# Kernel tuning notes

Measured on AMD Instinct MI355X. Metric: run time of the kernel, lower is better.

Reference implementation:

```python
import jax, jax.numpy as jnp
import numpy as np

B, T, E = 2, 2048, 1024   # batch, block_size, emb_d
H, D = 16, 64             # heads, head_size


def setup_inputs() -> dict:
    key = jax.random.key(0)
    ks = jax.random.split(key, 7)
    s = 1.0 / np.sqrt(E)
    inputs = jax.random.normal(ks[0], (B, T, E), dtype=jnp.float32)
    k_w = jax.random.uniform(ks[1], (H, E, D), jnp.float32, -s, s)
    k_b = jax.random.uniform(ks[2], (H, D), jnp.float32, -s, s)
    q_w = jax.random.uniform(ks[3], (H, E, D), jnp.float32, -s, s)
    q_b = jax.random.uniform(ks[4], (H, D), jnp.float32, -s, s)
    v_w = jax.random.uniform(ks[5], (H, E, D), jnp.float32, -s, s)
    v_b = jax.random.uniform(ks[6], (H, D), jnp.float32, -s, s)
    return {"inputs": inputs, "k_w": k_w, "k_b": k_b,
            "q_w": q_w, "q_b": q_b, "v_w": v_w, "v_b": v_b}


def reference(inputs, k_w, k_b, q_w, q_b, v_w, v_b):
    # Per-head linear projections, vectorized over heads: (B,T,E)x(H,E,D)->(B,H,T,D)
    k = jnp.einsum('bte,hed->bhtd', inputs, k_w) + k_b[None, :, None, :]
    q = jnp.einsum('bte,hed->bhtd', inputs, q_w) + q_b[None, :, None, :]
    v = jnp.einsum('bte,hed->bhtd', inputs, v_w) + v_b[None, :, None, :]

    scale = D ** (-0.5)
    # scores: (B,H,Tq,Tk)
    w = jnp.einsum('bhtd,bhsd->bhts', q, k) * scale
    tril = jnp.tril(jnp.ones((T, T), dtype=bool))
    w = jnp.where(tril[None, None, :, :], w, -jnp.inf)
    # NOTE: original torch code does softmax(weights, dim=1) on a (B,T,T)
    # tensor, i.e. over the QUERY axis. Faithfully reproduce: axis=-2 here.
    w = jax.nn.softmax(w, axis=-2)
    out = jnp.einsum('bhts,bhsd->bhtd', w, v)           # (B,H,T,D)
    # concat heads along last dim, head-major order matching torch.cat
    return out.transpose(0, 2, 1, 3).reshape(B, T, H * D)
```

## Files before the change

kernel.cpp:

```cpp
#include <hip/hip_runtime.h>
#include <hip/hip_bf16.h>
#include <math.h>

#define B_ 2
#define T_ 2048
#define E_ 1024
#define H_ 16
#define D_ 64
#define NT_ 32
#define QSCALE 0.180336880f

typedef __attribute__((ext_vector_type(8))) short bf16x8;
typedef __attribute__((ext_vector_type(4))) float f32x4;

#if __has_builtin(__builtin_amdgcn_exp2f)
#define EXP2(x) __builtin_amdgcn_exp2f(x)
#else
#define EXP2(x) exp2f(x)
#endif

__device__ __forceinline__ unsigned short f2bf(float x) {
  union { float f; unsigned u; } v; v.f = x;
  unsigned r = v.u + 0x7FFFu + ((v.u >> 16) & 1u);
  return (unsigned short)(r >> 16);
}
__device__ __forceinline__ unsigned pk2bf(float a, float b) {
  __hip_bfloat162 h = __float22bfloat162_rn(make_float2(a, b));
  union { __hip_bfloat162 h; unsigned u; } c; c.h = h; return c.u;
}

__device__ __forceinline__ void dma8(const unsigned short* g, int gstride,
                                     unsigned short* l, int lane)
{
  const int r = lane >> 3, bg = (lane & 7) ^ (r & 7);
  __builtin_amdgcn_global_load_lds(
      (const __attribute__((address_space(1))) void*)(g + (size_t)r * gstride + bg * 8),
      (__attribute__((address_space(3))) void*)l, 16, 0, 0);
}
__device__ __forceinline__ bf16x8 frag(const unsigned short* tile, int row, int g) {
  return *(const bf16x8*)(tile + row * 64 + (((g ^ row) & 7) << 3));
}

__global__ __launch_bounds__(256) void pack_kernel(
    const float* __restrict__ in, unsigned short* __restrict__ o16,
    const float* __restrict__ qw, const float* __restrict__ kw, const float* __restrict__ vw,
    unsigned short* __restrict__ qwt, unsigned short* __restrict__ kwt,
    unsigned short* __restrict__ vwt)
{
  __shared__ float s[64][65];
  const int tid = threadIdx.x;
  if (blockIdx.x < 2048) {
    const size_t i = ((size_t)blockIdx.x * 256 + tid) * 8;
    float4 f0 = *(const float4*)(in + i);
    float4 f1 = *(const float4*)(in + i + 4);
    unsigned u[4] = { pk2bf(f0.x, f0.y), pk2bf(f0.z, f0.w),
                      pk2bf(f1.x, f1.y), pk2bf(f1.z, f1.w) };
    *(bf16x8*)(o16 + i) = *(const bf16x8*)u;
    return;
  }
  const int i = blockIdx.x - 2048;
  const int e0 = (i & 15) * 64, h = (i >> 4) & 15, z = i >> 8;
  const float* w = (z == 0) ? qw : (z == 1) ? kw : vw;
  unsigned short* o = (z == 0) ? qwt : (z == 1) ? kwt : vwt;
  {
    const int r = tid >> 2;
    #pragma unroll
    for (int p = 0; p < 4; ++p) {
      const int c = (tid & 3) * 4 + p * 16;
      float4 f = *(const float4*)(w + ((size_t)(h * E_ + e0 + r)) * D_ + c);
      s[r][c] = f.x; s[r][c+1] = f.y; s[r][c+2] = f.z; s[r][c+3] = f.w;
    }
  }
  __syncthreads();
  {
    const int d = tid >> 2, ec = (tid & 3) * 16;
    unsigned short tmp[16];
    #pragma unroll
    for (int j = 0; j < 16; ++j) tmp[j] = f2bf(s[ec + j][d]);
    unsigned short* dst = o + ((size_t)(h * D_ + d)) * E_ + e0 + ec;
    *(bf16x8*)(dst)     = *(const bf16x8*)&tmp[0];
    *(bf16x8*)(dst + 8) = *(const bf16x8*)&tmp[8];
  }
}

__global__ __launch_bounds__(256) void proj_kernel(
    const unsigned short* __restrict__ in16,
    const unsigned short* __restrict__ qwt, const unsigned short* __restrict__ kwt,
    const unsigned short* __restrict__ vwt,
    const float* __restrict__ qb, const float* __restrict__ kb, const float* __restrict__ vb,
    unsigned short* __restrict__ qo, unsigned short* __restrict__ ko,
    unsigned short* __restrict__ vt)
{
  __shared__ __align__(16) unsigned short in_s[2][128 * 64];
  __shared__ __align__(16) unsigned short w_s[2][3 * 64 * 64];
  const int tid = threadIdx.x;
  const int lane = tid & 63, wv = tid >> 6;
  const int l15 = lane & 15, quad = lane >> 4;
  const int t0 = blockIdx.x * 128, h = blockIdx.y, b = blockIdx.z;
  const int bh = b * H_ + h;
  const unsigned short* wts[3] = { qwt, kwt, vwt };

  f32x4 acc[3][8];
  #pragma unroll
  for (int x = 0; x < 3; ++x)
    #pragma unroll
    for (int tb = 0; tb < 8; ++tb) acc[x][tb] = (f32x4){0.f, 0.f, 0.f, 0.f};

#define PROJ_STAGE(e0_, bi_)                                                      \
  {                                                                               \
    const unsigned short* gin = in16 + ((size_t)(b * T_ + t0)) * E_ + (e0_);      \
    _Pragma("unroll")                                                             \
    for (int p = 0; p < 4; ++p) {                                                 \
      const int br = wv * 32 + p * 8;                                             \
      dma8(gin + (size_t)br * E_, E_, &in_s[bi_][br * 64], lane);                 \
    }                                                                             \
    _Pragma("unroll")                                                             \
    for (int j = 0; j < 6; ++j) {                                                 \
      const int idx = wv * 6 + j;                                                 \
      const int x = idx >> 3, br = (idx & 7) * 8;                                 \
      dma8(wts[x] + ((size_t)(h * D_ + br)) * E_ + (e0_), E_,                     \
           &w_s[bi_][x * 4096 + br * 64], lane);                                  \
    }                                                                             \
  }

  PROJ_STAGE(0, 0);
  __syncthreads();
  for (int e = 0; e < 16; ++e) {
    const int bi = e & 1;
    if (e < 15) PROJ_STAGE((e + 1) * 64, bi ^ 1);
    const unsigned short* is = in_s[bi];
    const unsigned short* ws = w_s[bi];
    #pragma unroll
    for (int kk = 0; kk < 2; ++kk) {
      const int g0 = kk * 4 + quad;
      bf16x8 bfr[3];
      #pragma unroll
      for (int x = 0; x < 3; ++x)
        bfr[x] = frag(ws, x * 64 + wv * 16 + l15, g0);
      bf16x8 afr[8];
      #pragma unroll
      for (int tb = 0; tb < 8; ++tb)
        afr[tb] = frag(is, tb * 16 + l15, g0);
      #pragma unroll
      for (int tb = 0; tb < 8; ++tb) {
        acc[0][tb] = __builtin_amdgcn_mfma_f32_16x16x32_bf16(bfr[0], afr[tb], acc[0][tb], 0, 0, 0);
        acc[1][tb] = __builtin_amdgcn_mfma_f32_16x16x32_bf16(bfr[1], afr[tb], acc[1][tb], 0, 0, 0);
        acc[2][tb] = __builtin_amdgcn_mfma_f32_16x16x32_bf16(afr[tb], bfr[2], acc[2][tb], 0, 0, 0);
      }
    }
    __syncthreads();
  }
#undef PROJ_STAGE

  const size_t obase = (size_t)bh * T_;
  #pragma unroll
  for (int x = 0; x < 2; ++x) {
    const float scl = (x == 0) ? QSCALE : 1.0f;
    const float* bias = (x == 0) ? qb : kb;
    unsigned short* outp = (x == 0) ? qo : ko;
    float bias4[4];
    *(float4*)bias4 = *(const float4*)&bias[h * D_ + wv * 16 + quad * 4];
    #pragma unroll
    for (int tb = 0; tb < 8; ++tb) {
      const int t = t0 + tb * 16 + l15;
      unsigned short pk[4];
      #pragma unroll
      for (int r = 0; r < 4; ++r) pk[r] = f2bf((acc[x][tb][r] + bias4[r]) * scl);
      *(ushort4*)(outp + (obase + t) * D_ + wv * 16 + quad * 4) = *(const ushort4*)pk;
    }
  }
  {
    const int d = wv * 16 + l15;
    const float bvv = vb[h * D_ + d];
    #pragma unroll
    for (int tb = 0; tb < 8; ++tb) {
      const int t = t0 + tb * 16 + quad * 4;
      unsigned short pk[4];
      #pragma unroll
      for (int r = 0; r < 4; ++r) pk[r] = f2bf(acc[2][tb][r] + bvv);
      *(ushort4*)(vt + ((size_t)(bh * D_ + d)) * T_ + t) = *(const ushort4*)pk;
    }
  }
}

__global__ __launch_bounds__(256) void stats_kernel(
    const unsigned short* __restrict__ q, const unsigned short* __restrict__ k,
    float* __restrict__ lg)
{
  __shared__ __align__(16) unsigned short q_s[2][64 * 64];
  __shared__ float red[4][64];
  const int tid = threadIdx.x;
  const int lane = tid & 63, wv = tid >> 6;
  const int l15 = lane & 15, quad = lane >> 4;
  const int h = blockIdx.x, b = blockIdx.y, sa = blockIdx.z;
  const int bh = b * H_ + h;
  const int s0 = sa * 64;
  const unsigned short* qbase = q + (size_t)bh * T_ * 64;

  bf16x8 kf[4][2];
  #pragma unroll
  for (int nb = 0; nb < 4; ++nb)
    #pragma unroll
    for (int kk = 0; kk < 2; ++kk)
      kf[nb][kk] = *(const bf16x8*)(k + ((size_t)(bh * T_ + s0 + nb * 16 + l15)) * 64
                                      + kk * 32 + quad * 8);

  #pragma unroll
  for (int pp = 0; pp < 2; ++pp) {
    const int br = wv * 16 + pp * 8;
    dma8(qbase + (size_t)(sa * 64 + br) * 64, 64, &q_s[0][br * 64], lane);
  }
  __syncthreads();

  float lsum[4] = {0.f, 0.f, 0.f, 0.f};

  for (int tt = sa, i = 0; tt < NT_; ++tt, ++i) {
    const int bi = i & 1;
    if (tt + 1 < NT_) {
      #pragma unroll
      for (int pp = 0; pp < 2; ++pp) {
        const int br = wv * 16 + pp * 8;
        dma8(qbase + (size_t)((tt + 1) * 64 + br) * 64, 64, &q_s[bi ^ 1][br * 64], lane);
      }
    }
    bf16x8 a0 = frag(q_s[bi], wv * 16 + l15, quad);
    bf16x8 a1 = frag(q_s[bi], wv * 16 + l15, 4 + quad);
    f32x4 sacc[4];
    #pragma unroll
    for (int nb = 0; nb < 4; ++nb) sacc[nb] = (f32x4){0.f, 0.f, 0.f, 0.f};
    #pragma unroll
    for (int nb = 0; nb < 4; ++nb) {
      sacc[nb] = __builtin_amdgcn_mfma_f32_16x16x32_bf16(a0, kf[nb][0], sacc[nb], 0, 0, 0);
      sacc[nb] = __builtin_amdgcn_mfma_f32_16x16x32_bf16(a1, kf[nb][1], sacc[nb], 0, 0, 0);
    }
    if (tt == sa) {
      const int tbase = tt * 64 + wv * 16 + quad * 4;
      #pragma unroll
      for (int nb = 0; nb < 4; ++nb) {
        const int s = s0 + nb * 16 + l15;
        #pragma unroll
        for (int r = 0; r < 4; ++r)
          lsum[nb] += (tbase + r >= s) ? EXP2(sacc[nb][r]) : 0.f;
      }
    } else {
      #pragma unroll
      for (int nb = 0; nb < 4; ++nb)
        #pragma unroll
        for (int r = 0; r < 4; ++r) lsum[nb] += EXP2(sacc[nb][r]);
    }
    __syncthreads();
  }
  #pragma unroll
  for (int nb = 0; nb < 4; ++nb) {
    lsum[nb] += __shfl_xor(lsum[nb], 16);
    lsum[nb] += __shfl_xor(lsum[nb], 32);
  }
  if (lane < 16) {
    #pragma unroll
    for (int nb = 0; nb < 4; ++nb) red[wv][nb * 16 + lane] = lsum[nb];
  }
  __syncthreads();
  if (tid < 64) {
    const float L = red[0][tid] + red[1][tid] + red[2][tid] + red[3][tid];
    lg[(size_t)bh * T_ + s0 + tid] = -__log2f(L);
  }
}

__global__ __launch_bounds__(256) void out_kernel(
    const unsigned short* __restrict__ q, const unsigned short* __restrict__ k,
    const unsigned short* __restrict__ vt, const float* __restrict__ lg,
    float* __restrict__ out)
{
  __shared__ __align__(16) unsigned short k_s[2][64 * 64];
  __shared__ __align__(16) unsigned short vt_s[2][64 * 64];
  __shared__ __align__(16) unsigned short u_s[4][32][40];
  __shared__ float lg_sh[2][64];
  const int tid = threadIdx.x;
  const int lane = tid & 63, wv = tid >> 6;
  const int l15 = lane & 15, quad = lane >> 4;
  const int th = wv >> 1, sh = wv & 1;
  const int h = blockIdx.x, b = blockIdx.y, jt = 31 - blockIdx.z;
  const int bh = b * H_ + h;
  const int t0 = jt * 64;
  const unsigned short* kbase = k + (size_t)bh * T_ * 64;
  const unsigned short* vbase = vt + (size_t)bh * D_ * T_;
  const float* lgbase = lg + (size_t)bh * T_;

  bf16x8 qf[2][2];
  #pragma unroll
  for (int nt = 0; nt < 2; ++nt) {
    const unsigned short* qrow = q + (size_t)(bh * T_ + t0 + th * 32 + nt * 16 + l15) * 64;
    qf[nt][0] = *(const bf16x8*)(qrow + quad * 8);
    qf[nt][1] = *(const bf16x8*)(qrow + 32 + quad * 8);
  }

  #pragma unroll
  for (int pp = 0; pp < 2; ++pp) {
    const int br = wv * 16 + pp * 8;
    dma8(kbase + (size_t)br * 64, 64, &k_s[0][br * 64], lane);
    dma8(vbase + (size_t)br * T_, T_, &vt_s[0][br * 64], lane);
  }
  if (tid < 64) lg_sh[0][tid] = lgbase[tid];
  __syncthreads();

  f32x4 oacc[4][2];
  #pragma unroll
  for (int mb = 0; mb < 4; ++mb)
    #pragma unroll
    for (int nt = 0; nt < 2; ++nt) oacc[mb][nt] = (f32x4){0.f, 0.f, 0.f, 0.f};

  for (int st = 0; st <= jt; ++st) {
    const int bi = st & 1;
    if (st < jt) {
      const int s1 = (st + 1) * 64;
      #pragma unroll
      for (int pp = 0; pp < 2; ++pp) {
        const int br = wv * 16 + pp * 8;
        dma8(kbase + (size_t)(s1 + br) * 64, 64, &k_s[bi ^ 1][br * 64], lane);
        dma8(vbase + (size_t)br * T_ + s1, T_, &vt_s[bi ^ 1][br * 64], lane);
      }
      if (tid < 64) lg_sh[bi ^ 1][tid] = lgbase[s1 + tid];
    }
    const unsigned short* ks = k_s[bi];
    const unsigned short* vs = vt_s[bi];
    const float* lgb = lg_sh[bi];

    const bool dead = (st == jt) && (th == 0) && (sh == 1);
    if (!dead) {
      f32x4 sacc[2][2];
      #pragma unroll
      for (int mb = 0; mb < 2; ++mb) {
        float lg4[4];
        *(float4*)lg4 = *(const float4*)&lgb[sh * 32 + mb * 16 + quad * 4];
        #pragma unroll
        for (int nt = 0; nt < 2; ++nt)
          sacc[mb][nt] = (f32x4){lg4[0], lg4[1], lg4[2], lg4[3]};
      }
      #pragma unroll
      for (int mb = 0; mb < 2; ++mb) {
        bf16x8 ka0 = frag(ks, sh * 32 + mb * 16 + l15, quad);
        bf16x8 ka1 = frag(ks, sh * 32 + mb * 16 + l15, 4 + quad);
        #pragma unroll
        for (int nt = 0; nt < 2; ++nt) {
          sacc[mb][nt] = __builtin_amdgcn_mfma_f32_16x16x32_bf16(ka0, qf[nt][0], sacc[mb][nt], 0, 0, 0);
          sacc[mb][nt] = __builtin_amdgcn_mfma_f32_16x16x32_bf16(ka1, qf[nt][1], sacc[mb][nt], 0, 0, 0);
        }
      }
      const bool diagmask = (st == jt) && (th == sh);
      #pragma unroll
      for (int mb = 0; mb < 2; ++mb)
        #pragma unroll
        for (int nt = 0; nt < 2; ++nt) {
          float uu[4] = { EXP2(sacc[mb][nt][0]), EXP2(sacc[mb][nt][1]),
                          EXP2(sacc[mb][nt][2]), EXP2(sacc[mb][nt][3]) };
          if (diagmask) {
            const int tl = nt * 16 + l15, sl = mb * 16 + quad * 4;
            #pragma unroll
            for (int r = 0; r < 4; ++r) if (tl < sl + r) uu[r] = 0.f;
          }
          *(uint2*)(&u_s[wv][nt * 16 + l15][mb * 16 + quad * 4]) =
              make_uint2(pk2bf(uu[0], uu[1]), pk2bf(uu[2], uu[3]));
        }
      #pragma unroll
      for (int nt = 0; nt < 2; ++nt) {
        bf16x8 ua = *(const bf16x8*)(&u_s[wv][nt * 16 + l15][quad * 8]);
        #pragma unroll
        for (int mb = 0; mb < 4; ++mb)
          oacc[mb][nt] = __builtin_amdgcn_mfma_f32_16x16x32_bf16(
              frag(vs, mb * 16 + l15, sh * 4 + quad), ua, oacc[mb][nt], 0, 0, 0);
      }
    }
    __syncthreads();
  }

  float* scr = (float*)k_s;
  if (sh == 1) {
    #pragma unroll
    for (int mb = 0; mb < 4; ++mb)
      #pragma unroll
      for (int nt = 0; nt < 2; ++nt) {
        float o4[4] = { oacc[mb][nt][0], oacc[mb][nt][1], oacc[mb][nt][2], oacc[mb][nt][3] };
        *(float4*)&scr[((th * 8 + mb * 2 + nt) * 64 + lane) * 4] = *(const float4*)o4;
      }
  }
  __syncthreads();
  if (sh == 0) {
    #pragma unroll
    for (int nt = 0; nt < 2; ++nt) {
      float* orow = out + ((size_t)(b * T_ + t0 + th * 32 + nt * 16 + l15)) * (H_ * D_) + h * D_;
      #pragma unroll
      for (int mb = 0; mb < 4; ++mb) {
        float4 p = *(const float4*)&scr[((th * 8 + mb * 2 + nt) * 64 + lane) * 4];
        float o4[4] = { oacc[mb][nt][0] + p.x, oacc[mb][nt][1] + p.y,
                        oacc[mb][nt][2] + p.z, oacc[mb][nt][3] + p.w };
        *(float4*)(orow + mb * 16 + quad * 4) = *(const float4*)o4;
      }
    }
  }
}

extern "C" void kernel_launch(void* const* d_in, const int* in_sizes, int n_in,
                              void* d_out, int out_size, void* d_ws, size_t ws_size,
                              hipStream_t stream) {
  const float* in = (const float*)d_in[0];
  const float* kw = (const float*)d_in[1];
  const float* kb = (const float*)d_in[2];
  const float* qw = (const float*)d_in[3];
  const float* qb = (const float*)d_in[4];
  const float* vw = (const float*)d_in[5];
  const float* vb = (const float*)d_in[6];
  float* out = (float*)d_out;

  unsigned short* p = (unsigned short*)d_ws;
  const size_t inz = (size_t)B_ * T_ * E_;
  const size_t wz  = (size_t)H_ * D_ * E_;
  const size_t qz  = (size_t)B_ * H_ * T_ * D_;
  unsigned short* in16 = p;            p += inz;
  unsigned short* qwt  = p;            p += wz;
  unsigned short* kwt  = p;            p += wz;
  unsigned short* vwt  = p;            p += wz;
  unsigned short* q16  = p;            p += qz;
  unsigned short* k16  = p;            p += qz;
  unsigned short* vtb  = p;            p += qz;
  float* lgbuf = (float*)p;

  dim3 blk(256);
  pack_kernel <<<dim3(2048 + 768), blk, 0, stream>>>(in, in16, qw, kw, vw, qwt, kwt, vwt);
  proj_kernel <<<dim3(T_ / 128, H_, B_), blk, 0, stream>>>(in16, qwt, kwt, vwt,
                                                           qb, kb, vb, q16, k16, vtb);
  stats_kernel<<<dim3(H_, B_, NT_), blk, 0, stream>>>(q16, k16, lgbuf);
  out_kernel  <<<dim3(H_, B_, NT_), blk, 0, stream>>>(q16, k16, vtb, lgbuf, out);
}
```

Before: 169.9 us.

## Triple-buffer attention kernels with explicit waitcnt and direct-register projection weights

Converts the proj, stats and out kernels from double-buffered LDS staging to three-slot rings. Each iteration uses explicit vmcnt waits and a single barrier in place of a trailing __syncthreads. proj_kernel now loads weight fragments straight into registers (ping-pong) instead of staging them through LDS, and remaps the grid to a 1D launch with swizzled head order for L2 locality. out_kernel preloads the whole log-sum row into LDS and raises wave priority around the MFMA blocks. The hand-written vmcnt counts depend on the exact number of outstanding DMA ops, which is fragile if the compiler reorders loads.

```diff
diff --git a/kernel.cpp b/kernel.cpp
--- a/kernel.cpp
+++ b/kernel.cpp
@@ -83,7 +83,7 @@
   }
 }
 
-__global__ __launch_bounds__(256) void proj_kernel(
+__global__ __launch_bounds__(256, 3) void proj_kernel(
     const unsigned short* __restrict__ in16,
     const unsigned short* __restrict__ qwt, const unsigned short* __restrict__ kwt,
     const unsigned short* __restrict__ vwt,
@@ -91,14 +91,21 @@
     unsigned short* __restrict__ qo, unsigned short* __restrict__ ko,
     unsigned short* __restrict__ vt)
 {
-  __shared__ __align__(16) unsigned short in_s[2][128 * 64];
-  __shared__ __align__(16) unsigned short w_s[2][3 * 64 * 64];
+  __shared__ __align__(16) unsigned short in_s[3][128 * 64];
   const int tid = threadIdx.x;
   const int lane = tid & 63, wv = tid >> 6;
   const int l15 = lane & 15, quad = lane >> 4;
-  const int t0 = blockIdx.x * 128, h = blockIdx.y, b = blockIdx.z;
+  const int lin = blockIdx.x;
+  const int h = ((lin & 7) << 1) | ((lin >> 3) & 1);
+  const int rem = lin >> 4;
+  const int t0 = (rem & 15) * 128, b = rem >> 4;
   const int bh = b * H_ + h;
-  const unsigned short* wts[3] = { qwt, kwt, vwt };
+
+  const unsigned short* gin = in16 + ((size_t)(b * T_ + t0)) * E_;
+  const size_t wrow = ((size_t)(h * D_ + wv * 16 + l15)) * E_ + quad * 8;
+  const unsigned short* wp0 = qwt + wrow;
+  const unsigned short* wp1 = kwt + wrow;
+  const unsigned short* wp2 = vwt + wrow;
 
   f32x4 acc[3][8];
   #pragma unroll
@@ -106,51 +113,55 @@
     #pragma unroll
     for (int tb = 0; tb < 8; ++tb) acc[x][tb] = (f32x4){0.f, 0.f, 0.f, 0.f};
 
-#define PROJ_STAGE(e0_, bi_)                                                      \
-  {                                                                               \
-    const unsigned short* gin = in16 + ((size_t)(b * T_ + t0)) * E_ + (e0_);      \
-    _Pragma("unroll")                                                             \
-    for (int p = 0; p < 4; ++p) {                                                 \
-      const int br = wv * 32 + p * 8;                                             \
-      dma8(gin + (size_t)br * E_, E_, &in_s[bi_][br * 64], lane);                 \
-    }                                                                             \
-    _Pragma("unroll")                                                             \
-    for (int j = 0; j < 6; ++j) {                                                 \
-      const int idx = wv * 6 + j;                                                 \
-      const int x = idx >> 3, br = (idx & 7) * 8;                                 \
-      dma8(wts[x] + ((size_t)(h * D_ + br)) * E_ + (e0_), E_,                     \
-           &w_s[bi_][x * 4096 + br * 64], lane);                                  \
-    }                                                                             \
-  }
-
-  PROJ_STAGE(0, 0);
-  __syncthreads();
-  for (int e = 0; e < 16; ++e) {
-    const int bi = e & 1;
-    if (e < 15) PROJ_STAGE((e + 1) * 64, bi ^ 1);
-    const unsigned short* is = in_s[bi];
-    const unsigned short* ws = w_s[bi];
-    #pragma unroll
-    for (int kk = 0; kk < 2; ++kk) {
-      const int g0 = kk * 4 + quad;
-      bf16x8 bfr[3];
-      #pragma unroll
-      for (int x = 0; x < 3; ++x)
-        bfr[x] = frag(ws, x * 64 + wv * 16 + l15, g0);
-      bf16x8 afr[8];
-      #pragma unroll
-      for (int tb = 0; tb < 8; ++tb)
-        afr[tb] = frag(is, tb * 16 + l15, g0);
-      #pragma unroll
-      for (int tb = 0; tb < 8; ++tb) {
-        acc[0][tb] = __builtin_amdgcn_mfma_f32_16x16x32_bf16(bfr[0], afr[tb], acc[0][tb], 0, 0, 0);
-        acc[1][tb] = __builtin_amdgcn_mfma_f32_16x16x32_bf16(bfr[1], afr[tb], acc[1][tb], 0, 0, 0);
-        acc[2][tb] = __builtin_amdgcn_mfma_f32_16x16x32_bf16(afr[tb], bfr[2], acc[2][tb], 0, 0, 0);
-      }
-    }
-    __syncthreads();
-  }
-#undef PROJ_STAGE
+  bf16x8 wA[3][2], wB[3][2];
+
+#define P_STAGE(eoff_, slot_)                                                \
+  { const unsigned short* g_ = gin + (eoff_);                                \
+    _Pragma("unroll")                                                        \
+    for (int p = 0; p < 4; ++p) {                                            \
+      const int br = wv * 32 + p * 8;                                        \
+      dma8(g_ + (size_t)br * E_, E_, &in_s[slot_][br * 64], lane);           \
+    } }
+#define P_LOADW(e_, W)                                                       \
+  { W[0][0] = *(const bf16x8*)(wp0 + (e_) * 64);                             \
+    W[0][1] = *(const bf16x8*)(wp0 + (e_) * 64 + 32);                        \
+    W[1][0] = *(const bf16x8*)(wp1 + (e_) * 64);                             \
+    W[1][1] = *(const bf16x8*)(wp1 + (e_) * 64 + 32);                        \
+    W[2][0] = *(const bf16x8*)(wp2 + (e_) * 64);                             \
+    W[2][1] = *(const bf16x8*)(wp2 + (e_) * 64 + 32); }
+
+#define P_BODY(e_, WC, WN)                                                   \
+  { if ((e_) == 15) asm volatile("s_waitcnt vmcnt(6)" ::: "memory");         \
+    else            asm volatile("s_waitcnt vmcnt(10)" ::: "memory");        \
+    __builtin_amdgcn_s_barrier();                                            \
+    if ((e_) + 2 < 16) P_STAGE(((e_) + 2) * 64, ((e_) + 2) % 3);             \
+    if ((e_) + 1 < 16) P_LOADW((e_) + 1, WN);                                \
+    const unsigned short* is_ = in_s[(e_) % 3];                              \
+    __builtin_amdgcn_s_setprio(1);                                           \
+    _Pragma("unroll")                                                        \
+    for (int kk = 0; kk < 2; ++kk) {                                         \
+      _Pragma("unroll")                                                      \
+      for (int tb = 0; tb < 8; ++tb) {                                       \
+        bf16x8 a_ = frag(is_, tb * 16 + l15, kk * 4 + quad);                 \
+        acc[0][tb] = __builtin_amdgcn_mfma_f32_16x16x32_bf16(WC[0][kk], a_, acc[0][tb], 0, 0, 0); \
+        acc[1][tb] = __builtin_amdgcn_mfma_f32_16x16x32_bf16(WC[1][kk], a_, acc[1][tb], 0, 0, 0); \
+        acc[2][tb] = __builtin_amdgcn_mfma_f32_16x16x32_bf16(a_, WC[2][kk], acc[2][tb], 0, 0, 0); \
+      }                                                                      \
+    }                                                                        \
+    __builtin_amdgcn_s_setprio(0); }
+
+  P_STAGE(0, 0);
+  P_STAGE(64, 1);
+  P_LOADW(0, wA);
+  __syncthreads();
+
+  for (int e2 = 0; e2 < 16; e2 += 2) {
+    P_BODY(e2, wA, wB);
+    P_BODY(e2 + 1, wB, wA);
+  }
+#undef P_BODY
+#undef P_LOADW
+#undef P_STAGE
 
   const size_t obase = (size_t)bh * T_;
   #pragma unroll
@@ -187,7 +198,7 @@
     const unsigned short* __restrict__ q, const unsigned short* __restrict__ k,
     float* __restrict__ lg)
 {
-  __shared__ __align__(16) unsigned short q_s[2][64 * 64];
+  __shared__ __align__(16) unsigned short q_s[3][64 * 64];
   __shared__ float red[4][64];
   const int tid = threadIdx.x;
   const int lane = tid & 63, wv = tid >> 6;
@@ -205,26 +216,29 @@
       kf[nb][kk] = *(const bf16x8*)(k + ((size_t)(bh * T_ + s0 + nb * 16 + l15)) * 64
                                       + kk * 32 + quad * 8);
 
-  #pragma unroll
-  for (int pp = 0; pp < 2; ++pp) {
-    const int br = wv * 16 + pp * 8;
-    dma8(qbase + (size_t)(sa * 64 + br) * 64, 64, &q_s[0][br * 64], lane);
-  }
+#define ST_STAGE(tt_, slot_)                                                 \
+  { _Pragma("unroll")                                                        \
+    for (int pp = 0; pp < 2; ++pp) {                                         \
+      const int br = wv * 16 + pp * 8;                                       \
+      dma8(qbase + (size_t)((tt_) * 64 + br) * 64, 64, &q_s[slot_][br * 64], lane); \
+    } }
+
+  ST_STAGE(sa, 0);
+  if (sa + 1 < NT_) ST_STAGE(sa + 1, 1);
   __syncthreads();
 
   float lsum[4] = {0.f, 0.f, 0.f, 0.f};
 
-  for (int tt = sa, i = 0; tt < NT_; ++tt, ++i) {
-    const int bi = i & 1;
-    if (tt + 1 < NT_) {
-      #pragma unroll
-      for (int pp = 0; pp < 2; ++pp) {
-        const int br = wv * 16 + pp * 8;
-        dma8(qbase + (size_t)((tt + 1) * 64 + br) * 64, 64, &q_s[bi ^ 1][br * 64], lane);
-      }
-    }
-    bf16x8 a0 = frag(q_s[bi], wv * 16 + l15, quad);
-    bf16x8 a1 = frag(q_s[bi], wv * 16 + l15, 4 + quad);
+  for (int tt = sa; tt < NT_; ++tt) {
+    const int i = tt - sa;
+    if (tt < NT_ - 1) asm volatile("s_waitcnt vmcnt(2)" ::: "memory");
+    else              asm volatile("s_waitcnt vmcnt(0)" ::: "memory");
+    __builtin_amdgcn_s_barrier();
+    if (tt + 2 < NT_) ST_STAGE(tt + 2, (i + 2) % 3);
+
+    const unsigned short* qs = q_s[i % 3];
+    bf16x8 a0 = frag(qs, wv * 16 + l15, quad);
+    bf16x8 a1 = frag(qs, wv * 16 + l15, 4 + quad);
     f32x4 sacc[4];
     #pragma unroll
     for (int nb = 0; nb < 4; ++nb) sacc[nb] = (f32x4){0.f, 0.f, 0.f, 0.f};
@@ -248,8 +262,8 @@
         #pragma unroll
         for (int r = 0; r < 4; ++r) lsum[nb] += EXP2(sacc[nb][r]);
     }
-    __syncthreads();
-  }
+  }
+#undef ST_STAGE
   #pragma unroll
   for (int nb = 0; nb < 4; ++nb) {
     lsum[nb] += __shfl_xor(lsum[nb], 16);
@@ -271,10 +285,10 @@
     const unsigned short* __restrict__ vt, const float* __restrict__ lg,
     float* __restrict__ out)
 {
-  __shared__ __align__(16) unsigned short k_s[2][64 * 64];
-  __shared__ __align__(16) unsigned short vt_s[2][64 * 64];
+  __shared__ __align__(16) unsigned short k_s[3][64 * 64];
+  __shared__ __align__(16) unsigned short vt_s[3][64 * 64];
   __shared__ __align__(16) unsigned short u_s[4][32][40];
-  __shared__ float lg_sh[2][64];
+  __shared__ float lg_s[T_];
   const int tid = threadIdx.x;
   const int lane = tid & 63, wv = tid >> 6;
   const int l15 = lane & 15, quad = lane >> 4;
@@ -294,13 +308,20 @@
     qf[nt][1] = *(const bf16x8*)(qrow + 32 + quad * 8);
   }
 
-  #pragma unroll
-  for (int pp = 0; pp < 2; ++pp) {
-    const int br = wv * 16 + pp * 8;
-    dma8(kbase + (size_t)br * 64, 64, &k_s[0][br * 64], lane);
-    dma8(vbase + (size_t)br * T_, T_, &vt_s[0][br * 64], lane);
-  }
-  if (tid < 64) lg_sh[0][tid] = lgbase[tid];
+#define OUT_STAGE(soff_, slot_)                                              \
+  { _Pragma("unroll")                                                        \
+    for (int pp = 0; pp < 2; ++pp) {                                         \
+      const int br = wv * 16 + pp * 8;                                       \
+      dma8(kbase + (size_t)((soff_) + br) * 64, 64, &k_s[slot_][br * 64], lane); \
+      dma8(vbase + (size_t)br * T_ + (soff_), T_, &vt_s[slot_][br * 64], lane);  \
+    } }
+
+  const int lgn = (jt + 1) * 64;
+  for (int i = tid * 4; i < lgn; i += 1024)
+    *(float4*)&lg_s[i] = *(const float4*)&lgbase[i];
+
+  OUT_STAGE(0, 0);
+  if (jt >= 1) OUT_STAGE(64, 1);
   __syncthreads();
 
   f32x4 oacc[4][2];
@@ -310,20 +331,14 @@
     for (int nt = 0; nt < 2; ++nt) oacc[mb][nt] = (f32x4){0.f, 0.f, 0.f, 0.f};
 
   for (int st = 0; st <= jt; ++st) {
-    const int bi = st & 1;
-    if (st < jt) {
-      const int s1 = (st + 1) * 64;
-      #pragma unroll
-      for (int pp = 0; pp < 2; ++pp) {
-        const int br = wv * 16 + pp * 8;
-        dma8(kbase + (size_t)(s1 + br) * 64, 64, &k_s[bi ^ 1][br * 64], lane);
-        dma8(vbase + (size_t)br * T_ + s1, T_, &vt_s[bi ^ 1][br * 64], lane);
-      }
-      if (tid < 64) lg_sh[bi ^ 1][tid] = lgbase[s1 + tid];
-    }
-    const unsigned short* ks = k_s[bi];
-    const unsigned short* vs = vt_s[bi];
-    const float* lgb = lg_sh[bi];
+    if (st < jt) asm volatile("s_waitcnt vmcnt(4)" ::: "memory");
+    else         asm volatile("s_waitcnt vmcnt(0)" ::: "memory");
+    __builtin_amdgcn_s_barrier();
+    if (st + 2 <= jt) OUT_STAGE((st + 2) * 64, (st + 2) % 3);
+
+    const unsigned short* ks = k_s[st % 3];
+    const unsigned short* vs = vt_s[st % 3];
+    const float* lgb = &lg_s[st * 64];
 
     const bool dead = (st == jt) && (th == 0) && (sh == 1);
     if (!dead) {
@@ -336,6 +351,7 @@
         for (int nt = 0; nt < 2; ++nt)
           sacc[mb][nt] = (f32x4){lg4[0], lg4[1], lg4[2], lg4[3]};
       }
+      __builtin_amdgcn_s_setprio(1);
       #pragma unroll
       for (int mb = 0; mb < 2; ++mb) {
         bf16x8 ka0 = frag(ks, sh * 32 + mb * 16 + l15, quad);
@@ -346,6 +362,7 @@
           sacc[mb][nt] = __builtin_amdgcn_mfma_f32_16x16x32_bf16(ka1, qf[nt][1], sacc[mb][nt], 0, 0, 0);
         }
       }
+      __builtin_amdgcn_s_setprio(0);
       const bool diagmask = (st == jt) && (th == sh);
       #pragma unroll
       for (int mb = 0; mb < 2; ++mb)
@@ -361,6 +378,7 @@
           *(uint2*)(&u_s[wv][nt * 16 + l15][mb * 16 + quad * 4]) =
               make_uint2(pk2bf(uu[0], uu[1]), pk2bf(uu[2], uu[3]));
         }
+      __builtin_amdgcn_s_setprio(1);
       #pragma unroll
       for (int nt = 0; nt < 2; ++nt) {
         bf16x8 ua = *(const bf16x8*)(&u_s[wv][nt * 16 + l15][quad * 8]);
@@ -369,9 +387,11 @@
           oacc[mb][nt] = __builtin_amdgcn_mfma_f32_16x16x32_bf16(
               frag(vs, mb * 16 + l15, sh * 4 + quad), ua, oacc[mb][nt], 0, 0, 0);
       }
-    }
-    __syncthreads();
-  }
+      __builtin_amdgcn_s_setprio(0);
+    }
+  }
+#undef OUT_STAGE
+  __syncthreads();
 
   float* scr = (float*)k_s;
   if (sh == 1) {
@@ -426,8 +446,8 @@
 
   dim3 blk(256);
   pack_kernel <<<dim3(2048 + 768), blk, 0, stream>>>(in, in16, qw, kw, vw, qwt, kwt, vwt);
-  proj_kernel <<<dim3(T_ / 128, H_, B_), blk, 0, stream>>>(in16, qwt, kwt, vwt,
-                                                           qb, kb, vb, q16, k16, vtb);
+  proj_kernel <<<dim3(512), blk, 0, stream>>>(in16, qwt, kwt, vwt,
+                                              qb, kb, vb, q16, k16, vtb);
   stats_kernel<<<dim3(H_, B_, NT_), blk, 0, stream>>>(q16, k16, lgbuf);
   out_kernel  <<<dim3(H_, B_, NT_), blk, 0, stream>>>(q16, k16, vtb, lgbuf, out);
 }
```

Result: slower. 241.2 us (+41.9%).

## Load projection weights directly into registers and remap block order for locality

Applied to the files above, without the earlier changes.

The projection kernel no longer stages Q/K/V weights through shared memory. Each lane loads its weight fragments straight from global memory into double-buffered registers. Only the input tile is still staged via DMA, with a single barrier per step, manual vmcnt waits and raised wave priority around the MFMA loop. The grid is flattened to 1D with a swizzled head/time mapping intended to improve cache locality. This cuts LDS traffic and occupancy pressure but leans on the hand-tuned vmcnt count being correct.

```diff
diff --git a/kernel.cpp b/kernel.cpp
--- a/kernel.cpp
+++ b/kernel.cpp
@@ -92,13 +92,20 @@
     unsigned short* __restrict__ vt)
 {
   __shared__ __align__(16) unsigned short in_s[2][128 * 64];
-  __shared__ __align__(16) unsigned short w_s[2][3 * 64 * 64];
   const int tid = threadIdx.x;
   const int lane = tid & 63, wv = tid >> 6;
   const int l15 = lane & 15, quad = lane >> 4;
-  const int t0 = blockIdx.x * 128, h = blockIdx.y, b = blockIdx.z;
+  const int lin = blockIdx.x;
+  const int h = ((lin & 7) << 1) | ((lin >> 3) & 1);
+  const int rem = lin >> 4;
+  const int t0 = (rem & 15) * 128, b = rem >> 4;
   const int bh = b * H_ + h;
-  const unsigned short* wts[3] = { qwt, kwt, vwt };
+
+  const unsigned short* gin = in16 + ((size_t)(b * T_ + t0)) * E_;
+  const size_t wrow = ((size_t)(h * D_ + wv * 16 + l15)) * E_ + quad * 8;
+  const unsigned short* wp0 = qwt + wrow;
+  const unsigned short* wp1 = kwt + wrow;
+  const unsigned short* wp2 = vwt + wrow;
 
   f32x4 acc[3][8];
   #pragma unroll
@@ -106,51 +113,54 @@
     #pragma unroll
     for (int tb = 0; tb < 8; ++tb) acc[x][tb] = (f32x4){0.f, 0.f, 0.f, 0.f};
 
-#define PROJ_STAGE(e0_, bi_)                                                      \
-  {                                                                               \
-    const unsigned short* gin = in16 + ((size_t)(b * T_ + t0)) * E_ + (e0_);      \
-    _Pragma("unroll")                                                             \
-    for (int p = 0; p < 4; ++p) {                                                 \
-      const int br = wv * 32 + p * 8;                                             \
-      dma8(gin + (size_t)br * E_, E_, &in_s[bi_][br * 64], lane);                 \
-    }                                                                             \
-    _Pragma("unroll")                                                             \
-    for (int j = 0; j < 6; ++j) {                                                 \
-      const int idx = wv * 6 + j;                                                 \
-      const int x = idx >> 3, br = (idx & 7) * 8;                                 \
-      dma8(wts[x] + ((size_t)(h * D_ + br)) * E_ + (e0_), E_,                     \
-           &w_s[bi_][x * 4096 + br * 64], lane);                                  \
-    }                                                                             \
-  }
-
-  PROJ_STAGE(0, 0);
-  __syncthreads();
-  for (int e = 0; e < 16; ++e) {
-    const int bi = e & 1;
-    if (e < 15) PROJ_STAGE((e + 1) * 64, bi ^ 1);
-    const unsigned short* is = in_s[bi];
-    const unsigned short* ws = w_s[bi];
-    #pragma unroll
-    for (int kk = 0; kk < 2; ++kk) {
-      const int g0 = kk * 4 + quad;
-      bf16x8 bfr[3];
-      #pragma unroll
-      for (int x = 0; x < 3; ++x)
-        bfr[x] = frag(ws, x * 64 + wv * 16 + l15, g0);
-      bf16x8 afr[8];
-      #pragma unroll
-      for (int tb = 0; tb < 8; ++tb)
-        afr[tb] = frag(is, tb * 16 + l15, g0);
-      #pragma unroll
-      for (int tb = 0; tb < 8; ++tb) {
-        acc[0][tb] = __builtin_amdgcn_mfma_f32_16x16x32_bf16(bfr[0], afr[tb], acc[0][tb], 0, 0, 0);
-        acc[1][tb] = __builtin_amdgcn_mfma_f32_16x16x32_bf16(bfr[1], afr[tb], acc[1][tb], 0, 0, 0);
-        acc[2][tb] = __builtin_amdgcn_mfma_f32_16x16x32_bf16(afr[tb], bfr[2], acc[2][tb], 0, 0, 0);
-      }
-    }
-    __syncthreads();
-  }
-#undef PROJ_STAGE
+  bf16x8 wA[3][2], wB[3][2];
+
+#define P_STAGE(eoff_, slot_)                                                \
+  { const unsigned short* g_ = gin + (eoff_);                                \
+    _Pragma("unroll")                                                        \
+    for (int p = 0; p < 4; ++p) {                                            \
+      const int br = wv * 32 + p * 8;                                        \
+      dma8(g_ + (size_t)br * E_, E_, &in_s[slot_][br * 64], lane);           \
+    } }
+#define P_LOADW(e_, W)                                                       \
+  { W[0][0] = *(const bf16x8*)(wp0 + (e_) * 64);                             \
+    W[0][1] = *(const bf16x8*)(wp0 + (e_) * 64 + 32);                        \
+    W[1][0] = *(const bf16x8*)(wp1 + (e_) * 64);                             \
+    W[1][1] = *(const bf16x8*)(wp1 + (e_) * 64 + 32);                        \
+    W[2][0] = *(const bf16x8*)(wp2 + (e_) * 64);                             \
+    W[2][1] = *(const bf16x8*)(wp2 + (e_) * 64 + 32); }
+
+#define P_BODY(e_, WC, WN)                                                   \
+  { asm volatile("s_waitcnt vmcnt(6)" ::: "memory");                         \
+    __builtin_amdgcn_s_barrier();                                            \
+    if ((e_) + 1 < 16) {                                                     \
+      P_STAGE(((e_) + 1) * 64, ((e_) + 1) & 1);                              \
+      P_LOADW((e_) + 1, WN);                                                 \
+    }                                                                        \
+    const unsigned short* is_ = in_s[(e_) & 1];                              \
+    __builtin_amdgcn_s_setprio(1);                                           \
+    _Pragma("unroll")                                                        \
+    for (int kk = 0; kk < 2; ++kk) {                                         \
+      _Pragma("unroll")                                                      \
+      for (int tb = 0; tb < 8; ++tb) {                                       \
+        bf16x8 a_ = frag(is_, tb * 16 + l15, kk * 4 + quad);                 \
+        acc[0][tb] = __builtin_amdgcn_mfma_f32_16x16x32_bf16(WC[0][kk], a_, acc[0][tb], 0, 0, 0); \
+        acc[1][tb] = __builtin_amdgcn_mfma_f32_16x16x32_bf16(WC[1][kk], a_, acc[1][tb], 0, 0, 0); \
+        acc[2][tb] = __builtin_amdgcn_mfma_f32_16x16x32_bf16(a_, WC[2][kk], acc[2][tb], 0, 0, 0); \
+      }                                                                      \
+    }                                                                        \
+    __builtin_amdgcn_s_setprio(0); }
+
+  P_STAGE(0, 0);
+  P_LOADW(0, wA);
+
+  for (int e2 = 0; e2 < 16; e2 += 2) {
+    P_BODY(e2, wA, wB);
+    P_BODY(e2 + 1, wB, wA);
+  }
+#undef P_BODY
+#undef P_LOADW
+#undef P_STAGE
 
   const size_t obase = (size_t)bh * T_;
   #pragma unroll
@@ -426,8 +436,8 @@
 
   dim3 blk(256);
   pack_kernel <<<dim3(2048 + 768), blk, 0, stream>>>(in, in16, qw, kw, vw, qwt, kwt, vwt);
-  proj_kernel <<<dim3(T_ / 128, H_, B_), blk, 0, stream>>>(in16, qwt, kwt, vwt,
-                                                           qb, kb, vb, q16, k16, vtb);
+  proj_kernel <<<dim3(512), blk, 0, stream>>>(in16, qwt, kwt, vwt,
+                                              qb, kb, vb, q16, k16, vtb);
   stats_kernel<<<dim3(H_, B_, NT_), blk, 0, stream>>>(q16, k16, lgbuf);
   out_kernel  <<<dim3(H_, B_, NT_), blk, 0, stream>>>(q16, k16, vtb, lgbuf, out);
 }
```

Measured after the change: 189.5 us. 1.12x slower.

## Fuse stats and output kernels into one launch with atomic bitmask dependencies

Applied to the files above, without the earlier changes.

Merges the column-statistics kernel and the output kernel into a single launch. The first 1024 blocks compute the log-sum per key tile and publish completion through an atomic per-(batch,head) bitmask. The remaining blocks spin on that mask until every key tile they need is ready. This removes a kernel boundary and lets output blocks start while other stats blocks are still running. The cost is spin-wait overhead and a reliance on the lower-numbered stats blocks being scheduled first so the waiting blocks cannot deadlock.

```diff
diff --git a/kernel.cpp b/kernel.cpp
--- a/kernel.cpp
+++ b/kernel.cpp
@@ -45,10 +45,11 @@
     const float* __restrict__ in, unsigned short* __restrict__ o16,
     const float* __restrict__ qw, const float* __restrict__ kw, const float* __restrict__ vw,
     unsigned short* __restrict__ qwt, unsigned short* __restrict__ kwt,
-    unsigned short* __restrict__ vwt)
+    unsigned short* __restrict__ vwt, unsigned int* __restrict__ mask)
 {
   __shared__ float s[64][65];
   const int tid = threadIdx.x;
+  if (blockIdx.x == 0 && tid < 32) mask[tid] = 0;
   if (blockIdx.x < 2048) {
     const size_t i = ((size_t)blockIdx.x * 256 + tid) * 8;
     float4 f0 = *(const float4*)(in + i);
@@ -183,108 +184,121 @@
   }
 }
 
-__global__ __launch_bounds__(256) void stats_kernel(
+__global__ __launch_bounds__(256) void attn_kernel(
     const unsigned short* __restrict__ q, const unsigned short* __restrict__ k,
-    float* __restrict__ lg)
+    const unsigned short* __restrict__ vt, float* __restrict__ lg,
+    unsigned int* __restrict__ mask, float* __restrict__ out)
 {
-  __shared__ __align__(16) unsigned short q_s[2][64 * 64];
-  __shared__ float red[4][64];
+  __shared__ __align__(16) unsigned char smem[43520];
   const int tid = threadIdx.x;
   const int lane = tid & 63, wv = tid >> 6;
   const int l15 = lane & 15, quad = lane >> 4;
-  const int h = blockIdx.x, b = blockIdx.y, sa = blockIdx.z;
-  const int bh = b * H_ + h;
-  const int s0 = sa * 64;
-  const unsigned short* qbase = q + (size_t)bh * T_ * 64;
-
-  bf16x8 kf[4][2];
-  #pragma unroll
-  for (int nb = 0; nb < 4; ++nb)
-    #pragma unroll
-    for (int kk = 0; kk < 2; ++kk)
-      kf[nb][kk] = *(const bf16x8*)(k + ((size_t)(bh * T_ + s0 + nb * 16 + l15)) * 64
-                                      + kk * 32 + quad * 8);
-
-  #pragma unroll
-  for (int pp = 0; pp < 2; ++pp) {
-    const int br = wv * 16 + pp * 8;
-    dma8(qbase + (size_t)(sa * 64 + br) * 64, 64, &q_s[0][br * 64], lane);
-  }
-  __syncthreads();
-
-  float lsum[4] = {0.f, 0.f, 0.f, 0.f};
-
-  for (int tt = sa, i = 0; tt < NT_; ++tt, ++i) {
-    const int bi = i & 1;
-    if (tt + 1 < NT_) {
-      #pragma unroll
-      for (int pp = 0; pp < 2; ++pp) {
-        const int br = wv * 16 + pp * 8;
-        dma8(qbase + (size_t)((tt + 1) * 64 + br) * 64, 64, &q_s[bi ^ 1][br * 64], lane);
-      }
-    }
-    bf16x8 a0 = frag(q_s[bi], wv * 16 + l15, quad);
-    bf16x8 a1 = frag(q_s[bi], wv * 16 + l15, 4 + quad);
-    f32x4 sacc[4];
-    #pragma unroll
-    for (int nb = 0; nb < 4; ++nb) sacc[nb] = (f32x4){0.f, 0.f, 0.f, 0.f};
+  const int bidx = blockIdx.x;
+
+  if (bidx < 1024) {
+    unsigned short (*q_s)[64 * 64] = (unsigned short (*)[64 * 64])smem;
+    float (*red)[64] = (float (*)[64])(smem + 16384);
+    const int h = bidx & 15, b = (bidx >> 4) & 1, sa = bidx >> 5;
+    const int bh = b * H_ + h;
+    const int s0 = sa * 64;
+    const unsigned short* qbase = q + (size_t)bh * T_ * 64;
+
+    bf16x8 kf[4][2];
+    #pragma unroll
+    for (int nb = 0; nb < 4; ++nb)
+      #pragma unroll
+      for (int kk = 0; kk < 2; ++kk)
+        kf[nb][kk] = *(const bf16x8*)(k + ((size_t)(bh * T_ + s0 + nb * 16 + l15)) * 64
+                                        + kk * 32 + quad * 8);
+
+    #pragma unroll
+    for (int pp = 0; pp < 2; ++pp) {
+      const int br = wv * 16 + pp * 8;
+      dma8(qbase + (size_t)(sa * 64 + br) * 64, 64, &q_s[0][br * 64], lane);
+    }
+    __syncthreads();
+
+    float lsum[4] = {0.f, 0.f, 0.f, 0.f};
+
+    for (int tt = sa, i = 0; tt < NT_; ++tt, ++i) {
+      const int bi = i & 1;
+      if (tt + 1 < NT_) {
+        #pragma unroll
+        for (int pp = 0; pp < 2; ++pp) {
+          const int br = wv * 16 + pp * 8;
+          dma8(qbase + (size_t)((tt + 1) * 64 + br) * 64, 64, &q_s[bi ^ 1][br * 64], lane);
+        }
+      }
+      bf16x8 a0 = frag(q_s[bi], wv * 16 + l15, quad);
+      bf16x8 a1 = frag(q_s[bi], wv * 16 + l15, 4 + quad);
+      f32x4 sacc[4];
+      #pragma unroll
+      for (int nb = 0; nb < 4; ++nb) sacc[nb] = (f32x4){0.f, 0.f, 0.f, 0.f};
+      #pragma unroll
+      for (int nb = 0; nb < 4; ++nb) {
+        sacc[nb] = __builtin_amdgcn_mfma_f32_16x16x32_bf16(a0, kf[nb][0], sacc[nb], 0, 0, 0);
+        sacc[nb] = __builtin_amdgcn_mfma_f32_16x16x32_bf16(a1, kf[nb][1], sacc[nb], 0, 0, 0);
+      }
+      if (tt == sa) {
+        const int tbase = tt * 64 + wv * 16 + quad * 4;
+        #pragma unroll
+        for (int nb = 0; nb < 4; ++nb) {
+          const int s = s0 + nb * 16 + l15;
+          #pragma unroll
+          for (int r = 0; r < 4; ++r)
+            lsum[nb] += (tbase + r >= s) ? EXP2(sacc[nb][r]) : 0.f;
+        }
+      } else {
+        #pragma unroll
+        for (int nb = 0; nb < 4; ++nb)
+          #pragma unroll
+          for (int r = 0; r < 4; ++r) lsum[nb] += EXP2(sacc[nb][r]);
+      }
+      __syncthreads();
+    }
     #pragma unroll
     for (int nb = 0; nb < 4; ++nb) {
-      sacc[nb] = __builtin_amdgcn_mfma_f32_16x16x32_bf16(a0, kf[nb][0], sacc[nb], 0, 0, 0);
-      sacc[nb] = __builtin_amdgcn_mfma_f32_16x16x32_bf16(a1, kf[nb][1], sacc[nb], 0, 0, 0);
-    }
-    if (tt == sa) {
-      const int tbase = tt * 64 + wv * 16 + quad * 4;
-      #pragma unroll
-      for (int nb = 0; nb < 4; ++nb) {
-        const int s = s0 + nb * 16 + l15;
-        #pragma unroll
-        for (int r = 0; r < 4; ++r)
-          lsum[nb] += (tbase + r >= s) ? EXP2(sacc[nb][r]) : 0.f;
-      }
-    } else {
-      #pragma unroll
-      for (int nb = 0; nb < 4; ++nb)
-        #pragma unroll
-        for (int r = 0; r < 4; ++r) lsum[nb] += EXP2(sacc[nb][r]);
+      lsum[nb] += __shfl_xor(lsum[nb], 16);
+      lsum[nb] += __shfl_xor(lsum[nb], 32);
+    }
+    if (lane < 16) {
+      #pragma unroll
+      for (int nb = 0; nb < 4; ++nb) red[wv][nb * 16 + lane] = lsum[nb];
     }
     __syncthreads();
-  }
-  #pragma unroll
-  for (int nb = 0; nb < 4; ++nb) {
-    lsum[nb] += __shfl_xor(lsum[nb], 16);
-    lsum[nb] += __shfl_xor(lsum[nb], 32);
-  }
-  if (lane < 16) {
-    #pragma unroll
-    for (int nb = 0; nb < 4; ++nb) red[wv][nb * 16 + lane] = lsum[nb];
-  }
-  __syncthreads();
-  if (tid < 64) {
-    const float L = red[0][tid] + red[1][tid] + red[2][tid] + red[3][tid];
-    lg[(size_t)bh * T_ + s0 + tid] = -__log2f(L);
-  }
-}
-
-__global__ __launch_bounds__(256) void out_kernel(
-    const unsigned short* __restrict__ q, const unsigned short* __restrict__ k,
-    const unsigned short* __restrict__ vt, const float* __restrict__ lg,
-    float* __restrict__ out)
-{
-  __shared__ __align__(16) unsigned short k_s[2][64 * 64];
-  __shared__ __align__(16) unsigned short vt_s[2][64 * 64];
-  __shared__ __align__(16) unsigned short u_s[4][32][40];
-  __shared__ float lg_sh[2][64];
-  const int tid = threadIdx.x;
-  const int lane = tid & 63, wv = tid >> 6;
-  const int l15 = lane & 15, quad = lane >> 4;
+    if (tid < 64) {
+      const float L = red[0][tid] + red[1][tid] + red[2][tid] + red[3][tid];
+      __hip_atomic_store(&lg[(size_t)bh * T_ + s0 + tid], -__log2f(L),
+                         __ATOMIC_RELAXED, __HIP_MEMORY_SCOPE_AGENT);
+    }
+    __syncthreads();
+    if (tid == 0)
+      __hip_atomic_fetch_or(&mask[bh], 1u << sa, __ATOMIC_RELEASE,
+                            __HIP_MEMORY_SCOPE_AGENT);
+    return;
+  }
+
+  unsigned short (*k_s)[4096]  = (unsigned short (*)[4096])smem;
+  unsigned short (*vt_s)[4096] = (unsigned short (*)[4096])(smem + 16384);
+  unsigned short (*u_s)[32][40] = (unsigned short (*)[32][40])(smem + 32768);
+  float (*lg_sh)[64] = (float (*)[64])(smem + 43008);
+
+  const int j = bidx - 1024;
+  const int h = j & 15, b = (j >> 4) & 1, jt = 31 - (j >> 5);
   const int th = wv >> 1, sh = wv & 1;
-  const int h = blockIdx.x, b = blockIdx.y, jt = 31 - blockIdx.z;
   const int bh = b * H_ + h;
   const int t0 = jt * 64;
   const unsigned short* kbase = k + (size_t)bh * T_ * 64;
   const unsigned short* vbase = vt + (size_t)bh * D_ * T_;
   const float* lgbase = lg + (size_t)bh * T_;
+
+  if (tid == 0) {
+    const unsigned need = (jt >= 31) ? 0xFFFFFFFFu : ((2u << jt) - 1u);
+    while ((__hip_atomic_load(&mask[bh], __ATOMIC_ACQUIRE,
+                              __HIP_MEMORY_SCOPE_AGENT) & need) != need)
+      __builtin_amdgcn_s_sleep(8);
+  }
+  __syncthreads();
 
   bf16x8 qf[2][2];
   #pragma unroll
@@ -300,7 +314,9 @@
     dma8(kbase + (size_t)br * 64, 64, &k_s[0][br * 64], lane);
     dma8(vbase + (size_t)br * T_, T_, &vt_s[0][br * 64], lane);
   }
-  if (tid < 64) lg_sh[0][tid] = lgbase[tid];
+  if (tid < 64)
+    lg_sh[0][tid] = __hip_atomic_load(&lgbase[tid], __ATOMIC_RELAXED,
+                                      __HIP_MEMORY_SCOPE_AGENT);
   __syncthreads();
 
   f32x4 oacc[4][2];
@@ -319,7 +335,9 @@
         dma8(kbase + (size_t)(s1 + br) * 64, 64, &k_s[bi ^ 1][br * 64], lane);
         dma8(vbase + (size_t)br * T_ + s1, T_, &vt_s[bi ^ 1][br * 64], lane);
       }
-      if (tid < 64) lg_sh[bi ^ 1][tid] = lgbase[s1 + tid];
+      if (tid < 64)
+        lg_sh[bi ^ 1][tid] = __hip_atomic_load(&lgbase[s1 + tid], __ATOMIC_RELAXED,
+                                               __HIP_MEMORY_SCOPE_AGENT);
     }
     const unsigned short* ks = k_s[bi];
     const unsigned short* vs = vt_s[bi];
@@ -423,11 +441,12 @@
   unsigned short* k16  = p;            p += qz;
   unsigned short* vtb  = p;            p += qz;
   float* lgbuf = (float*)p;
+  unsigned int* maskbuf = (unsigned int*)(lgbuf + (size_t)B_ * H_ * T_);
 
   dim3 blk(256);
-  pack_kernel <<<dim3(2048 + 768), blk, 0, stream>>>(in, in16, qw, kw, vw, qwt, kwt, vwt);
+  pack_kernel <<<dim3(2048 + 768), blk, 0, stream>>>(in, in16, qw, kw, vw,
+                                                     qwt, kwt, vwt, maskbuf);
   proj_kernel <<<dim3(T_ / 128, H_, B_), blk, 0, stream>>>(in16, qwt, kwt, vwt,
                                                            qb, kb, vb, q16, k16, vtb);
-  stats_kernel<<<dim3(H_, B_, NT_), blk, 0, stream>>>(q16, k16, lgbuf);
-  out_kernel  <<<dim3(H_, B_, NT_), blk, 0, stream>>>(q16, k16, vtb, lgbuf, out);
-}
+  attn_kernel <<<dim3(2048), blk, 0, stream>>>(q16, k16, vtb, lgbuf, maskbuf, out);
+}
```

Result: slower. 246.5 us (+45.1%).
